# Performance work log

Hardware: AMD Instinct MI355X
Metric: run time of the kernel (lower is better)

Reference implementation:

```python
import jax, jax.numpy as jnp
import numpy as np

N = 2048
H_DIM = 64
N_HEADS = 4
N_HIDDEN = H_DIM // N_HEADS  # is_concat=True
L = 16  # max_labels_dim
SLOPE = 0.2


def leaky(x, slope=SLOPE):
    return jnp.where(x >= 0, x, slope * x)


def setup_inputs() -> dict:
    key = jax.random.key(0)
    k1, k2, k3, k4 = jax.random.split(key, 4)
    x = jax.random.normal(k1, (N, H_DIM), dtype=jnp.float32)
    # labels in [0, L]; value == L means unlabeled -> all-zero one-hot row
    lab = jax.random.randint(k2, (N,), 0, L + 1)
    ohm_labels = jnp.where((lab < L)[:, None],
                           jax.nn.one_hot(jnp.minimum(lab, L - 1), L, dtype=jnp.float32),
                           0.0)
    in_features = H_DIM + L
    W_l = jax.random.normal(k3, (H_DIM, in_features), dtype=jnp.float32) / np.sqrt(in_features)
    W_attn = jax.random.normal(k4, (N_HIDDEN,), dtype=jnp.float32) / np.sqrt(N_HIDDEN)
    return {"x": x, "ohm_labels": ohm_labels, "W_l": W_l, "W_attn": W_attn, "sparsity": 0}


def reference(x, ohm_labels, W_l, W_attn, sparsity):
    n_nodes = x.shape[0]
    # fill unlabeled rows with uniform 1/L
    unlabeled = ohm_labels.sum(axis=1) == 0  # (N,)
    ohm = jnp.where(unlabeled[:, None], 1.0 / L, ohm_labels)
    pin = jnp.concatenate([x, ohm], axis=1)  # (N, h_dim + L)

    # shared-weight projection: g_l == g_r == g
    g = (pin @ W_l.T).reshape(n_nodes, N_HEADS, N_HIDDEN)  # (N, H, F)
    # g_sum[i, j] = g_l[j] + g_r[i]  (repeat / repeat_interleave semantics)
    g_sum = g[None, :, :, :] + g[:, None, :, :]            # (N, N, H, F)
    e = jnp.einsum('ijhf,f->ijh', leaky(g_sum), W_attn)    # (N, N, H)
    a = jax.nn.softmax(e, axis=1)                          # softmax over j
    # dropout in eval mode: identity
    attn_res = jnp.einsum('ijh,jhf->ihf', a, g)            # (N, H, F)
    out = attn_res.reshape(n_nodes, N_HEADS * N_HIDDEN)    # is_concat
    h = leaky(out)                                         # processor activation

    # centroids per label from ohm (post-fill) as in get_centroids
    cluster_agg = ohm.T @ h                                # (L, D)
    cnt = ohm.sum(axis=0)                                  # (L,)
    missing = cnt == 0
    centroids = jnp.where(missing[:, None], 0.0,
                          cluster_agg / jnp.where(missing, 1.0, cnt)[:, None])
    # cdist p=2
    diff = h[:, None, :] - centroids[None, :, :]           # (N, L, D)
    scores = -jnp.sqrt(jnp.sum(diff * diff, axis=-1))      # (N, L)
    return scores, h, missing
```

## Files before the change

kernel.cpp:

```cpp
#include <hip/hip_runtime.h>
#include <hip/hip_bf16.h>
#include <math.h>

#define C1F  0.577078016f
#define C2F  0.865617024f

#define WS_CNT 0
#define WS_AGG 128
#define WS_G   8320
#define WS_DCL (8320 + 524288)

typedef float __attribute__((ext_vector_type(4))) f32x4;

__device__ __forceinline__ float rfl(float x) {
    return __uint_as_float(__builtin_amdgcn_readfirstlane(__float_as_uint(x)));
}

__device__ __forceinline__ float dpp_sum(float x) {
    float y;
    y = __int_as_float(__builtin_amdgcn_update_dpp(0, __float_as_int(x), 0x111, 0xf, 0xf, true)); x += y;
    y = __int_as_float(__builtin_amdgcn_update_dpp(0, __float_as_int(x), 0x112, 0xf, 0xf, true)); x += y;
    y = __int_as_float(__builtin_amdgcn_update_dpp(0, __float_as_int(x), 0x114, 0xf, 0xf, true)); x += y;
    y = __int_as_float(__builtin_amdgcn_update_dpp(0, __float_as_int(x), 0x118, 0xf, 0xf, true)); x += y;
    y = __int_as_float(__builtin_amdgcn_update_dpp(0, __float_as_int(x), 0x142, 0xa, 0xf, true)); x += y;
    y = __int_as_float(__builtin_amdgcn_update_dpp(0, __float_as_int(x), 0x143, 0xc, 0xf, true)); x += y;
    return x;
}

__global__ __launch_bounds__(256) void k_proj(
    const float* __restrict__ x, const float* __restrict__ ohm,
    const float* __restrict__ Wl, const float* __restrict__ Wattn,
    unsigned char* __restrict__ ws)
{
    float* g2   = (float*)(ws + WS_G);
    float* dclT = (float*)(ws + WS_DCL);
    unsigned long long* cnt = (unsigned long long*)(ws + WS_CNT);

    int t = threadIdx.x;
    int r = blockIdx.x * 4 + (t >> 6);
    int o = t & 63;

    f32x4 oh[4]; float rs = 0.f;
    const f32x4* ohp = (const f32x4*)&ohm[r*16];
    #pragma unroll
    for (int q = 0; q < 4; ++q) { oh[q] = ohp[q]; rs += oh[q][0]+oh[q][1]+oh[q][2]+oh[q][3]; }
    if (rs == 0.f) {
        f32x4 c = {0.0625f, 0.0625f, 0.0625f, 0.0625f};
        #pragma unroll
        for (int q = 0; q < 4; ++q) oh[q] = c;
    }

    float acc = 0.f;
    const f32x4* xp = (const f32x4*)&x[r*64];
    const f32x4* wp = (const f32x4*)&Wl[o*80];
    #pragma unroll
    for (int q = 0; q < 16; ++q) {
        f32x4 a = xp[q], b = wp[q];
        acc = fmaf(a[0],b[0],acc); acc = fmaf(a[1],b[1],acc);
        acc = fmaf(a[2],b[2],acc); acc = fmaf(a[3],b[3],acc);
    }
    #pragma unroll
    for (int q = 0; q < 4; ++q) {
        f32x4 b = wp[16+q];
        acc = fmaf(oh[q][0],b[0],acc); acc = fmaf(oh[q][1],b[1],acc);
        acc = fmaf(oh[q][2],b[2],acc); acc = fmaf(oh[q][3],b[3],acc);
    }
    g2[(o >> 4)*32768 + (o & 15)*2048 + r] = acc;

    float dot = Wattn[o & 15] * acc;
    #pragma unroll
    for (int m2 = 1; m2 < 16; m2 <<= 1) dot += __shfl_xor(dot, m2);
    if ((o & 15) == 0) dclT[(o >> 4)*2048 + r] = C2F * dot;

    if (t < 16) {
        float c = 0.f;
        for (int rr = 0; rr < 4; ++rr) {
            int r2 = blockIdx.x*4 + rr; float s = 0.f;
            #pragma unroll
            for (int k = 0; k < 16; ++k) s += ohm[r2*16+k];
            c += (s == 0.f) ? 0.0625f : ohm[r2*16+t];
        }
        atomicAdd(&cnt[t], (unsigned long long)__float2ll_rn(c * 1048576.0f));
    }
}

__global__ __launch_bounds__(1024, 1) void k_attn(
    const float* __restrict__ ohm, const float* __restrict__ Wattn,
    unsigned char* __restrict__ ws, float* __restrict__ hout)
{
    float* g2   = (float*)(ws + WS_G);
    float* dclT = (float*)(ws + WS_DCL);
    unsigned long long* agg = (unsigned long long*)(ws + WS_AGG);

    __shared__ float g2l[16*2048];
    __shared__ float djl[2048];
    __shared__ float shh[32*16];
    __shared__ float ohmf[32*16];

    int t = threadIdx.x, bid = blockIdx.x;
    int h  = bid >> 6;
    int ib = (bid & 63) * 32;
    int wid = t >> 6, l = t & 63;
    int i0 = ib + wid*2, i1 = i0 + 1;

    const float* g2h = g2 + h*32768;
    const float* dph = dclT + h*2048;

    {
        const f32x4* s4 = (const f32x4*)g2h;
        f32x4* d4 = (f32x4*)g2l;
        #pragma unroll
        for (int c = 0; c < 8; ++c) d4[t + c*1024] = s4[t + c*1024];
        if (t < 512) ((f32x4*)djl)[t] = ((const f32x4*)dph)[t];
    }
    float wv[16], gA0[16], gA1[16];
    #pragma unroll
    for (int f = 0; f < 16; ++f) {
        wv[f]  = rfl(Wattn[f]);
        gA0[f] = rfl(g2h[f*2048 + i0]);
        gA1[f] = rfl(g2h[f*2048 + i1]);
    }
    __syncthreads();

    float acc0[16], acc1[16];
    float l0 = 0.f, l1 = 0.f;
    #pragma unroll
    for (int f = 0; f < 16; ++f) { acc0[f] = 0.f; acc1[f] = 0.f; }

    #pragma unroll 1
    for (int pass = 0; pass < 8; ++pass) {
        int pp = (pass + wid) & 7;
        int jb = pp*256 + 4*l;
        f32x4 G[16];
        #pragma unroll
        for (int f = 0; f < 16; ++f) G[f] = *(const f32x4*)&g2l[f*2048 + jb];
        f32x4 dj = *(const f32x4*)&djl[jb];

        float e00=0.f,e01=0.f,e02=0.f,e03=0.f;
        float e10=0.f,e11=0.f,e12=0.f,e13=0.f;
        #pragma unroll
        for (int f = 0; f < 16; ++f) {
            float a0 = gA0[f], a1 = gA1[f];
            f32x4 gf = G[f];
            e00 = fmaf(wv[f], fabsf(a0 + gf[0]), e00);
            e01 = fmaf(wv[f], fabsf(a0 + gf[1]), e01);
            e02 = fmaf(wv[f], fabsf(a0 + gf[2]), e02);
            e03 = fmaf(wv[f], fabsf(a0 + gf[3]), e03);
            e10 = fmaf(wv[f], fabsf(a1 + gf[0]), e10);
            e11 = fmaf(wv[f], fabsf(a1 + gf[1]), e11);
            e12 = fmaf(wv[f], fabsf(a1 + gf[2]), e12);
            e13 = fmaf(wv[f], fabsf(a1 + gf[3]), e13);
        }
        float p00 = __builtin_amdgcn_exp2f(fmaf(C1F, e00, dj[0]));
        float p01 = __builtin_amdgcn_exp2f(fmaf(C1F, e01, dj[1]));
        float p02 = __builtin_amdgcn_exp2f(fmaf(C1F, e02, dj[2]));
        float p03 = __builtin_amdgcn_exp2f(fmaf(C1F, e03, dj[3]));
        float p10 = __builtin_amdgcn_exp2f(fmaf(C1F, e10, dj[0]));
        float p11 = __builtin_amdgcn_exp2f(fmaf(C1F, e11, dj[1]));
        float p12 = __builtin_amdgcn_exp2f(fmaf(C1F, e12, dj[2]));
        float p13 = __builtin_amdgcn_exp2f(fmaf(C1F, e13, dj[3]));
        l0 += (p00 + p01) + (p02 + p03);
        l1 += (p10 + p11) + (p12 + p13);
        #pragma unroll
        for (int f = 0; f < 16; ++f) {
            f32x4 gf = G[f];
            acc0[f] = fmaf(p00, gf[0], fmaf(p01, gf[1],
                      fmaf(p02, gf[2], fmaf(p03, gf[3], acc0[f]))));
            acc1[f] = fmaf(p10, gf[0], fmaf(p11, gf[1],
                      fmaf(p12, gf[2], fmaf(p13, gf[3], acc1[f]))));
        }
    }

    float ls0 = dpp_sum(l0), ls1 = dpp_sum(l1);
    float h0[16], h1[16];
    #pragma unroll
    for (int f = 0; f < 16; ++f) { h0[f] = dpp_sum(acc0[f]); h1[f] = dpp_sum(acc1[f]); }

    if (l == 63) {
        float r0 = 1.0f / ls0, r1 = 1.0f / ls1;
        #pragma unroll
        for (int f = 0; f < 16; ++f) {
            float a = h0[f]*r0; a = fmaxf(a, 0.2f*a);
            float b = h1[f]*r1; b = fmaxf(b, 0.2f*b);
            hout[i0*64 + h*16 + f] = a;
            hout[i1*64 + h*16 + f] = b;
            shh[(wid*2    )*16 + f] = a;
            shh[(wid*2 + 1)*16 + f] = b;
        }
    }
    if (t < 512) {
        int r = t >> 4, lab = t & 15;
        float v = ohm[(ib + r)*16 + lab];
        float s = v;
        #pragma unroll
        for (int m2 = 1; m2 < 16; m2 <<= 1) s += __shfl_xor(s, m2);
        ohmf[r*16 + lab] = (s == 0.f) ? 0.0625f : v;
    }
    __syncthreads();

    if (t < 256) {
        int lab = t >> 4, dq = t & 15;
        float s = 0.f;
        #pragma unroll 8
        for (int r = 0; r < 32; ++r)
            s = fmaf(ohmf[r*16 + lab], shh[r*16 + dq], s);
        atomicAdd(&agg[lab*64 + h*16 + dq],
                  (unsigned long long)__float2ll_rn(s * 67108864.0f));
    }
}

__global__ __launch_bounds__(256) void k_scores(
    unsigned char* __restrict__ ws, const float* __restrict__ hout,
    float* __restrict__ scores, float* __restrict__ missing)
{
    __shared__ float cl[16*68];
    unsigned long long* cnt = (unsigned long long*)(ws + WS_CNT);
    unsigned long long* agg = (unsigned long long*)(ws + WS_AGG);
    int t = threadIdx.x;

    for (int v = t; v < 1024; v += 256) {
        int ll = v >> 6, d = v & 63;
        long long a = (long long)agg[v];
        long long c = (long long)cnt[ll];
        cl[ll*68 + d] = (c == 0) ? 0.f : ((float)a / (float)c) * 0.015625f;
    }
    if (blockIdx.x == 0 && t < 16) missing[t] = (cnt[t] == 0) ? 1.0f : 0.0f;
    __syncthreads();

    int i = blockIdx.x*16 + (t >> 4), ll = t & 15;
    float s = 0.f;
    #pragma unroll 16
    for (int d = 0; d < 64; ++d) {
        float diff = hout[i*64 + d] - cl[ll*68 + d];
        s = fmaf(diff, diff, s);
    }
    scores[i*16 + ll] = -sqrtf(s);
}

extern "C" void kernel_launch(void* const* d_in, const int* in_sizes, int n_in,
                              void* d_out, int out_size, void* d_ws, size_t ws_size,
                              hipStream_t stream)
{
    const float* x     = (const float*)d_in[0];
    const float* ohm   = (const float*)d_in[1];
    const float* Wl    = (const float*)d_in[2];
    const float* Wattn = (const float*)d_in[3];
    unsigned char* ws  = (unsigned char*)d_ws;

    float* out     = (float*)d_out;
    float* scores  = out;
    float* hout    = out + 2048*16;
    float* missing = out + 2048*16 + 2048*64;

    hipMemsetAsync(d_ws, 0, 8320, stream);
    k_proj  <<<512, 256, 0, stream>>>(x, ohm, Wl, Wattn, ws);
    k_attn  <<<256, 1024, 0, stream>>>(ohm, Wattn, ws, hout);
    k_scores<<<128, 256, 0, stream>>>(ws, hout, scores, missing);
}
```

Measured before the change: 54.74 us.

## Replace fixed-point global atomics with per-block partials reduced in scores kernel

The fixed-point 64-bit atomicAdd accumulation of label counts and per-label aggregates is replaced with per-block partial writes to workspace. The scores kernel then reduces these partials in float before computing centroids. This removes the memset launch and atomic contention on a few addresses. In exchange, every scores block redundantly re-reduces 256K floats of partials, which adds global reads.

```diff
diff --git a/kernel.cpp b/kernel.cpp
--- a/kernel.cpp
+++ b/kernel.cpp
@@ -5,10 +5,10 @@
 #define C1F  0.577078016f
 #define C2F  0.865617024f
 
-#define WS_CNT 0
-#define WS_AGG 128
-#define WS_G   8320
-#define WS_DCL (8320 + 524288)
+#define WS_CNTP 0
+#define WS_AGGP 32768
+#define WS_G    294912
+#define WS_DCL  819200
 
 typedef float __attribute__((ext_vector_type(4))) f32x4;
 
@@ -34,7 +34,7 @@
 {
     float* g2   = (float*)(ws + WS_G);
     float* dclT = (float*)(ws + WS_DCL);
-    unsigned long long* cnt = (unsigned long long*)(ws + WS_CNT);
+    float* cntp = (float*)(ws + WS_CNTP);
 
     int t = threadIdx.x;
     int r = blockIdx.x * 4 + (t >> 6);
@@ -80,7 +80,7 @@
             for (int k = 0; k < 16; ++k) s += ohm[r2*16+k];
             c += (s == 0.f) ? 0.0625f : ohm[r2*16+t];
         }
-        atomicAdd(&cnt[t], (unsigned long long)__float2ll_rn(c * 1048576.0f));
+        cntp[t*512 + blockIdx.x] = c;
     }
 }
 
@@ -90,7 +90,7 @@
 {
     float* g2   = (float*)(ws + WS_G);
     float* dclT = (float*)(ws + WS_DCL);
-    unsigned long long* agg = (unsigned long long*)(ws + WS_AGG);
+    float* aggp = (float*)(ws + WS_AGGP);
 
     __shared__ float g2l[16*2048];
     __shared__ float djl[2048];
@@ -99,7 +99,8 @@
 
     int t = threadIdx.x, bid = blockIdx.x;
     int h  = bid >> 6;
-    int ib = (bid & 63) * 32;
+    int rg = bid & 63;
+    int ib = rg * 32;
     int wid = t >> 6, l = t & 63;
     int i0 = ib + wid*2, i1 = i0 + 1;
 
@@ -204,8 +205,7 @@
         #pragma unroll 8
         for (int r = 0; r < 32; ++r)
             s = fmaf(ohmf[r*16 + lab], shh[r*16 + dq], s);
-        atomicAdd(&agg[lab*64 + h*16 + dq],
-                  (unsigned long long)__float2ll_rn(s * 67108864.0f));
+        aggp[h*16384 + (lab*16 + dq)*64 + rg] = s;
     }
 }
 
@@ -214,17 +214,34 @@
     float* __restrict__ scores, float* __restrict__ missing)
 {
     __shared__ float cl[16*68];
-    unsigned long long* cnt = (unsigned long long*)(ws + WS_CNT);
-    unsigned long long* agg = (unsigned long long*)(ws + WS_AGG);
+    __shared__ float scnt[16];
+    const float* cntp = (const float*)(ws + WS_CNTP);
+    const float* aggp = (const float*)(ws + WS_AGGP);
     int t = threadIdx.x;
 
+    if (t < 128) {
+        int lab = t >> 3, seg = t & 7;
+        const f32x4* p = (const f32x4*)&cntp[lab*512 + seg*64];
+        float c = 0.f;
+        #pragma unroll
+        for (int q = 0; q < 16; ++q) { f32x4 v = p[q]; c += (v[0]+v[1])+(v[2]+v[3]); }
+        #pragma unroll
+        for (int m2 = 1; m2 < 8; m2 <<= 1) c += __shfl_xor(c, m2);
+        if (seg == 0) scnt[lab] = c;
+    }
+    __syncthreads();
+
     for (int v = t; v < 1024; v += 256) {
-        int ll = v >> 6, d = v & 63;
-        long long a = (long long)agg[v];
-        long long c = (long long)cnt[ll];
-        cl[ll*68 + d] = (c == 0) ? 0.f : ((float)a / (float)c) * 0.015625f;
-    }
-    if (blockIdx.x == 0 && t < 16) missing[t] = (cnt[t] == 0) ? 1.0f : 0.0f;
+        int lab = v >> 6, d = v & 63;
+        int h = d >> 4, dq = d & 15;
+        const f32x4* p = (const f32x4*)&aggp[h*16384 + (lab*16 + dq)*64];
+        float a = 0.f;
+        #pragma unroll
+        for (int q = 0; q < 16; ++q) { f32x4 x4 = p[q]; a += (x4[0]+x4[1])+(x4[2]+x4[3]); }
+        float c = scnt[lab];
+        cl[lab*68 + d] = (c == 0.f) ? 0.f : a / c;
+    }
+    if (blockIdx.x == 0 && t < 16) missing[t] = (scnt[t] == 0.f) ? 1.0f : 0.0f;
     __syncthreads();
 
     int i = blockIdx.x*16 + (t >> 4), ll = t & 15;
@@ -252,7 +269,6 @@
     float* hout    = out + 2048*16;
     float* missing = out + 2048*16 + 2048*64;
 
-    hipMemsetAsync(d_ws, 0, 8320, stream);
     k_proj  <<<512, 256, 0, stream>>>(x, ohm, Wl, Wattn, ws);
     k_attn  <<<256, 1024, 0, stream>>>(ohm, Wattn, ws, hout);
     k_scores<<<128, 256, 0, stream>>>(ws, hout, scores, missing);
```

Result: no change. 53.89 us (-1.6%).
